# Performance work log

Measured on AMD Instinct MI355X. Metric: run time of the kernel, lower is better.

Reference implementation:

```python
import jax, jax.numpy as jnp
import numpy as np

B, L, SIZE, HEADS, AH, NBR, KER, DEPTH = 64, 512, 128, 8, 16, 15, 16, 3
MAXD = 20.0
N = B * L
EDGE = KER + 3 + 9 + 1  # 29


def _normalize(v):
    return v / (jnp.linalg.norm(v, axis=-1, keepdims=True) + 1e-8)


def _frames(pos):
    # local orientation frame per residue from consecutive CA displacements
    u = _normalize(pos[1:] - pos[:-1])            # (N-1,3)
    up = jnp.concatenate([u[:1], u], axis=0)      # u_{i-1}
    un = jnp.concatenate([u, u[-1:]], axis=0)     # u_i
    b = _normalize(up - un)
    n = _normalize(jnp.cross(up, un))
    return jnp.stack([b, n, jnp.cross(b, n)], axis=-1)  # (N,3,3)


def setup_inputs() -> dict:
    key = jax.random.key(0)
    ks = jax.random.split(key, 16)
    g = lambda i, shape, s=1.0: jax.random.normal(ks[i], shape, jnp.float32) * s
    return {
        "tertiary": g(0, (N, 3, 3), 10.0),
        "sequence": g(1, (N, 20)),
        "subgraph_indices": jnp.arange(N, dtype=jnp.int32) // L,
        "knn_noise": g(2, (B, L, L)),
        "embed_w": g(3, (27, SIZE), 0.1), "embed_b": jnp.zeros((SIZE,), jnp.float32),
        "wq": g(4, (DEPTH, SIZE, HEADS * AH), 0.08),
        "wk": g(5, (DEPTH, SIZE + EDGE, HEADS * AH), 0.08),
        "wv": g(6, (DEPTH, SIZE + EDGE, HEADS * AH), 0.08),
        "wo": g(7, (DEPTH, HEADS * AH, SIZE), 0.08),
        "mlp_w1": g(8, (DEPTH, SIZE, SIZE), 0.08), "mlp_b1": jnp.zeros((DEPTH, SIZE), jnp.float32),
        "mlp_w2": g(9, (DEPTH, SIZE, SIZE), 0.08), "mlp_b2": jnp.zeros((DEPTH, SIZE), jnp.float32),
        "mlp_w3": g(10, (DEPTH, SIZE, SIZE), 0.08), "mlp_b3": jnp.zeros((DEPTH, SIZE), jnp.float32),
        "pool_w": g(11, (4, SIZE, SIZE, 3), 0.05), "pool_b": jnp.zeros((4, SIZE), jnp.float32),
        "energy_w": g(12, (SIZE, 1), 0.1), "energy_b": jnp.zeros((1,), jnp.float32),
    }


def _forward(tertiary, sequence, knn_noise, embed_w, embed_b, wq, wk, wv, wo,
             mlp_w1, mlp_b1, mlp_w2, mlp_b2, mlp_w3, mlp_b3,
             pool_w, pool_b, energy_w, energy_b):
    pos = tertiary[:, 1]                                   # (N,3) CA positions
    R = _frames(pos)                                       # (N,3,3)
    # ---- kNN per contiguous protein group with noisy distances ----
    pg = pos.reshape(B, L, 3)
    dist = jnp.linalg.norm(pg[:, :, None] - pg[:, None, :], axis=-1)  # (B,L,L)
    closeness = -dist + 3.0 * knn_noise
    idx = jax.lax.top_k(closeness, NBR)[1]                 # (B,L,NBR) local
    nbr = (idx + (jnp.arange(B) * L)[:, None, None]).reshape(N, NBR)
    # ---- RBF relative encoding (RelativeStructure.message) ----
    dvec = pos[nbr] - pos[:, None]                         # (N,NBR,3)
    d = jnp.linalg.norm(dvec, axis=-1)                     # (N,NBR)
    mu = jnp.linspace(0.0, MAXD, KER)
    sigma = MAXD / KER
    rbf = jnp.exp(-(((d[..., None] - mu) / sigma) ** 2))   # (N,NBR,KER)
    dirs = jnp.einsum('nrc,nkr->nkc', R, dvec / (d[..., None] + 1e-8))
    relrot = jnp.einsum('nrc,nkrd->nkcd', R, R[nbr]).reshape(N, NBR, 9)
    ind = jnp.arange(N, dtype=tertiary.dtype)
    relind = (ind[nbr] - ind[:, None])[..., None]
    edge = jnp.concatenate([rbf, dirs, relrot, relind], axis=-1)  # (N,NBR,EDGE)
    # ---- structured graph-attention encoder ----
    h = jnp.ones((N, 27), tertiary.dtype) @ embed_w + embed_b
    inv_sqrt = 1.0 / np.sqrt(AH).astype(np.float32)
    for l in range(DEPTH):
        q = (h @ wq[l]).reshape(N, HEADS, AH)
        kv = jnp.concatenate([h[nbr], edge], axis=-1)      # (N,NBR,SIZE+EDGE)
        k = (kv @ wk[l]).reshape(N, NBR, HEADS, AH)
        v = (kv @ wv[l]).reshape(N, NBR, HEADS, AH)
        logits = jnp.einsum('nhd,nkhd->nhk', q, k) * inv_sqrt
        a = jax.nn.softmax(logits, axis=-1)
        o = jnp.einsum('nhk,nkhd->nhd', a, v).reshape(N, HEADS * AH) @ wo[l]
        h = h + o
        m = jax.nn.relu(h @ mlp_w1[l] + mlp_b1[l])
        m = jax.nn.relu(m @ mlp_w2[l] + mlp_b2[l])
        h = h + m @ mlp_w3[l] + mlp_b3[l]
    # ---- scatter-pad pool: residual conv + maxpool(2), x4, then length-sum ----
    x = h.reshape(B, L, SIZE).transpose(0, 2, 1)           # (B,SIZE,L)
    for i in range(4):
        y = jax.lax.conv_general_dilated(
            x, pool_w[i], (1,), ((1, 1),),
            dimension_numbers=('NCH', 'OIH', 'NCH')) + pool_b[i][None, :, None]
        x = x + jax.nn.leaky_relu(y, 0.01)
        Lc = x.shape[-1]
        x = x.reshape(B, SIZE, Lc // 2, 2).max(axis=-1)
    pooled = x.sum(axis=-1)                                # (B,SIZE)
    return pooled @ energy_w + energy_b                    # (B,1)


def reference(tertiary, sequence, subgraph_indices, knn_noise, embed_w, embed_b,
              wq, wk, wv, wo, mlp_w1, mlp_b1, mlp_w2, mlp_b2, mlp_w3, mlp_b3,
              pool_w, pool_b, energy_w, energy_b):
    # subgraph_indices encodes contiguous equal-size groups (arange // L)
    return _forward(tertiary, sequence, knn_noise, embed_w, embed_b, wq, wk, wv, wo,
                    mlp_w1, mlp_b1, mlp_w2, mlp_b2, mlp_w3, mlp_b3,
                    pool_w, pool_b, energy_w, energy_b)
```

## Files before the change

kernel.cpp:

```cpp
#include <hip/hip_runtime.h>
#include <math.h>

#define N_TOT 32768
#define NNBR 15
#define APW 8
#define ELPH 40
#define ETP 20
#define PLP 20

#define KNB 4096
#define FRB 128
#define PRB 3392

#define EB 1920

typedef __attribute__((ext_vector_type(8))) _Float16 f16x8;
typedef __attribute__((ext_vector_type(2))) _Float16 f16x2;
typedef __attribute__((ext_vector_type(4))) float f32x4;

#define CBAR() __asm__ volatile("" ::: "memory")
#define PAIR(v, c) __builtin_shufflevector(v, v, 2 * (c), 2 * (c) + 1)

__device__ __forceinline__ _Float16 f2h(float x) { return (_Float16)x; }

// ... 214 lines not shown
      int r = idx % 32768;
      int blk = r >> 14;
      int cout = (r >> 7) & 127;
      int jp = r & 127;
      int j = blk * 128 + jp;
      float val = 0.f;
      if (j < 232) {
        int e = j >> 3, hh = j & 7;
        const float* wvp = wv + (size_t)lL * 157 * 128 + (size_t)(128 + e) * 128 + hh * 16;
        const float* wop = wo + (size_t)lL * 16384 + (size_t)(hh * 16) * 128 + cout;
#pragma unroll
        for (int d = 0; d < 16; d++) val = fmaf(wvp[d], wop[d * 128], val);
      }
      wpe[(size_t)idx] = f2h(val);
    } else if (pb2 < 2880) {
      int idx = (pb2 - 2112) * 256 + tid;
      int kt = idx % 3;
      int rest = idx / 3;
      int i = rest % 128; rest /= 128;
      int oo = rest % 128;
      int s = rest / 128;
      wct[(((size_t)s * 3 + kt) * 128 + oo) * 128 + i] = f2h(pw[idx]);
    } else {
      int vb = pb2 - 2880;
      if (tid < 128) {
        float s = ebias[tid];
#pragma unroll
        for (int i = 0; i < 27; i++) s += ew[i * 128 + tid];
        hvS[tid] = s;
      }
      __syncthreads();
      size_t total = (size_t)N_TOT * 128;
      for (size_t j = (size_t)vb * 256 + tid; j < total; j += (size_t)512 * 256)
        h[j] = f2h(hvS[j & 127]);
    }
  }
}

template <int NTHR>
__device__ __forceinline__ void stage_w_async(const _Float16* __restrict__ W,
                                              _Float16* Ws, int tid) {
  int wv = tid >> 6, lane = tid & 63;
  constexpr int ITERS = 16384 / (NTHR * 8);
#pragma unroll
  for (int it = 0; it < ITERS; it++) {
    int base = it * (NTHR * 8) + wv * 512;
    int off = base + lane * 8;
    int row = off >> 7;
    int cL = (off >> 3) & 15;
    int cS = cL ^ (row & 7);
    const _Float16* src = W + ((size_t)row << 7) + (cS << 3);
    __builtin_amdgcn_global_load_lds(
        (const __attribute__((address_space(1))) void*)src,
        (__attribute__((address_space(3))) void*)(Ws + base), 16, 0, 0);
  }
}
template <int NTHR, int ROWS>
__device__ __forceinline__ void stage_x(const _Float16* __restrict__ src, _Float16* X,
                                        int tid, int rowstride) {
  for (int j = tid; j < ROWS * 16; j += NTHR) {
    int row = j >> 4, seg = (j & 15) * 8;
    *(uint4*)&X[row * 136 + seg] = *(const uint4*)(src + (size_t)row * rowstride + seg);
  }
}
template <bool RESET>
__device__ __forceinline__ void gemm_tile_t(const _Float16* X, const _Float16* Ws,
                                            int wrow, int l16, int quad, f32x4 acc[8]) {
  if (RESET) {
#pragma unroll
    for (int t = 0; t < 8; t++) acc[t] = (f32x4){0.f, 0.f, 0.f, 0.f};
  }
#pragma unroll
  for (int kk = 0; kk < 4; kk++) {
    f16x8 a = *(const f16x8*)&X[(wrow + l16) * 136 + kk * 32 + quad * 8];
#pragma unroll
    for (int t = 0; t < 8; t++) {
      int rw = t * 16 + l16;
      f16x8 b = *(const f16x8*)&Ws[(rw << 7) + ((((kk << 2) + quad) ^ (rw & 7)) << 3)];
      acc[t] = __builtin_amdgcn_mfma_f32_16x16x32_f16(a, b, acc[t], 0, 0, 0);
    }
  }
}

__global__ __launch_bounds__(256) void k_eq(const float* __restrict__ pos,
                                            const float* __restrict__ R,
                                            const int* __restrict__ nbr,
                                            _Float16* __restrict__ edge,
                                            const _Float16* __restrict__ A,
                                            const _Float16* __restrict__ Wqt,
                                            const _Float16* __restrict__ Wkt,
                                            const _Float16* __restrict__ Wvt,
                                            const _Float16* __restrict__ Wqk0,
                                            const _Float16* __restrict__ Wqk1,
                                            _Float16* __restrict__ q, _Float16* __restrict__ hk,
                                            _Float16* __restrict__ hv, _Float16* __restrict__ qkw) {
  __shared__ _Float16 X[64 * 136];
  __shared__ _Float16 Ws[128 * 128];
  int bb = blockIdx.x, tid = threadIdx.x;
  if (bb < EB) {
    int idx = bb * 256 + tid;
    if (idx >= N_TOT * NNBR) return;
    int n = idx / NNBR;
    int m = nbr[idx];
    float dx = pos[m * 3 + 0] - pos[n * 3 + 0];
    float dy = pos[m * 3 + 1] - pos[n * 3 + 1];
    float dz = pos[m * 3 + 2] - pos[n * 3 + 2];
    float d = sqrtf(dx * dx + dy * dy + dz * dz);
    _Float16 eb[32];
#pragma unroll
    for (int j = 0; j < 16; j++) {
      float mu = (20.f / 15.f) * (float)j;
      float t = (d - mu) * 0.8f;
      eb[j] = f2h(__expf(-t * t));
    }
    float inv = 1.f / (d + 1e-8f);
    float ux = dx * inv, uy = dy * inv, uz = dz * inv;
    float Rn[9], Rm[9];
#pragma unroll
    for (int j = 0; j < 9; j++) { Rn[j] = R[(size_t)n * 9 + j]; Rm[j] = R[(size_t)m * 9 + j]; }
#pragma unroll
    for (int cc = 0; cc < 3; cc++)
      eb[16 + cc] = f2h(Rn[0 * 3 + cc] * ux + Rn[1 * 3 + cc] * uy + Rn[2 * 3 + cc] * uz);
#pragma unroll
    for (int cc = 0; cc < 3; cc++)
#pragma unroll
      for (int dd = 0; dd < 3; dd++)
        eb[19 + cc * 3 + dd] = f2h(Rn[0 * 3 + cc] * Rm[0 * 3 + dd] +
                                   Rn[1 * 3 + cc] * Rm[1 * 3 + dd] +
                                   Rn[2 * 3 + cc] * Rm[2 * 3 + dd]);
    eb[28] = f2h((float)(m - n));
    eb[29] = (_Float16)0.f; eb[30] = (_Float16)0.f; eb[31] = (_Float16)0.f;
    _Float16* e = edge + (size_t)idx * 32;
#pragma unroll
    for (int v = 0; v < 4; v++)
      *(uint4*)(e + v * 8) = *(const uint4*)(&eb[v * 8]);
  } else {
    int r0 = (bb - EB) * 64;
    int lane = tid & 63, quad = lane >> 4, l16 = lane & 15, wrow = (tid >> 6) * 16;
    stage_x<256, 64>(A + (size_t)r0 * 128, X, tid, 128);
    const _Float16* wts[5] = {Wqt, Wkt, Wvt, Wqk0, Wqk1};
    f32x4 acc[8];
    for (int w = 0; w < 5; w++) {
      __syncthreads();
      stage_w_async<256>(wts[w], Ws, tid);
      __syncthreads();
      gemm_tile_t<true>(X, Ws, wrow, l16, quad, acc);
#pragma unroll
      for (int t = 0; t < 8; t++) {
        int col = t * 16 + l16;
#pragma unroll
        for (int r = 0; r < 4; r++) {
          float v = acc[t][r];
          int rowg = r0 + wrow + quad * 4 + r;
          if (w < 3) {
            _Float16* C = (w == 0) ? q : (w == 1) ? hk : hv;
            C[(size_t)rowg * 128 + col] = f2h(v);
          } else {
            qkw[(size_t)rowg * 256 + (w - 3) * 128 + col] = f2h(v);
          }
        }
      }
    }
  }
}

__global__ __launch_bounds__(256) void k_post(const _Float16* __restrict__ o,
                                              const _Float16* __restrict__ pe_g,
                                              _Float16* __restrict__ h,
                                              const _Float16* __restrict__ Wot,
                                              const _Float16* __restrict__ Wpe0,
                                              const _Float16* __restrict__ Wpe1,
                                              const _Float16* __restrict__ W1t, const float* __restrict__ B1,
                                              const _Float16* __restrict__ W2t, const float* __restrict__ B2,
                                              const _Float16* __restrict__ W3t, const float* __restrict__ B3,
                                              const _Float16* __restrict__ Wqt,
                                              const _Float16* __restrict__ Wkt,
                                              const _Float16* __restrict__ Wvt,
                                              const _Float16* __restrict__ Wqk0,
                                              const _Float16* __restrict__ Wqk1,
                                              _Float16* __restrict__ qo, _Float16* __restrict__ hko,
                                              _Float16* __restrict__ hvo, _Float16* __restrict__ qkwo,
                                              int do_qkv) {
  __shared__ _Float16 X[64 * 136];
  __shared__ _Float16 Ws[128 * 128];
  int tid = threadIdx.x, r0 = blockIdx.x * 64;
  int lane = tid & 63, quad = lane >> 4, l16 = lane & 15, wrow = (tid >> 6) * 16;
  f32x4 acc[8], hres[8];
  stage_x<256, 64>(o + (size_t)r0 * 128, X, tid, 128);
  stage_w_async<256>(Wot, Ws, tid);
  __syncthreads();
  gemm_tile_t<true>(X, Ws, wrow, l16, quad, acc);
  const _Float16* wpes[2] = {Wpe0, Wpe1};
#pragma unroll 1
  for (int blk = 0; blk < 2; blk++) {
    __syncthreads();
    stage_x<256, 64>(pe_g + (size_t)r0 * 256 + blk * 128, X, tid, 256);
    stage_w_async<256>(wpes[blk], Ws, tid);
    __syncthreads();
    gemm_tile_t<false>(X, Ws, wrow, l16, quad, acc);
  }
#pragma unroll
  for (int t = 0; t < 8; t++) {
    int col = t * 16 + l16;
#pragma unroll
    for (int r = 0; r < 4; r++)
      hres[t][r] = acc[t][r] + (float)h[(size_t)(r0 + wrow + quad * 4 + r) * 128 + col];
  }
  __syncthreads();
#pragma unroll
  for (int t = 0; t < 8; t++) {
    int col = t * 16 + l16;
#pragma unroll
    for (int r = 0; r < 4; r++)
      X[(wrow + quad * 4 + r) * 136 + col] = f2h(hres[t][r]);
  }
  stage_w_async<256>(W1t, Ws, tid);
  __syncthreads();
  gemm_tile_t<true>(X, Ws, wrow, l16, quad, acc);
  __syncthreads();
#pragma unroll
  for (int t = 0; t < 8; t++) {
    int col = t * 16 + l16; float bv = B1[col];
#pragma unroll
    for (int r = 0; r < 4; r++)
      X[(wrow + quad * 4 + r) * 136 + col] = f2h(fmaxf(acc[t][r] + bv, 0.f));
  }
  stage_w_async<256>(W2t, Ws, tid);
  __syncthreads();
  gemm_tile_t<true>(X, Ws, wrow, l16, quad, acc);
  __syncthreads();
#pragma unroll
  for (int t = 0; t < 8; t++) {
    int col = t * 16 + l16; float bv = B2[col];
#pragma unroll
    for (int r = 0; r < 4; r++)
      X[(wrow + quad * 4 + r) * 136 + col] = f2h(fmaxf(acc[t][r] + bv, 0.f));
  }
  stage_w_async<256>(W3t, Ws, tid);
  __syncthreads();
  gemm_tile_t<true>(X, Ws, wrow, l16, quad, acc);
  __syncthreads();
#pragma unroll
  for (int t = 0; t < 8; t++) {
    int col = t * 16 + l16; float bv = B3[col];
#pragma unroll
    for (int r = 0; r < 4; r++) {
      float v = hres[t][r] + acc[t][r] + bv;
      h[(size_t)(r0 + wrow + quad * 4 + r) * 128 + col] = f2h(v);
      if (do_qkv) X[(wrow + quad * 4 + r) * 136 + col] = f2h(v);
    }
  }
  if (!do_qkv) return;
  const _Float16* wts[5] = {Wqt, Wkt, Wvt, Wqk0, Wqk1};
  for (int w = 0; w < 5; w++) {
    __syncthreads();
    stage_w_async<256>(wts[w], Ws, tid);
    __syncthreads();
    gemm_tile_t<true>(X, Ws, wrow, l16, quad, acc);
#pragma unroll
    for (int t = 0; t < 8; t++) {
      int col = t * 16 + l16;
#pragma unroll
      for (int r = 0; r < 4; r++) {
        float v = acc[t][r];
        int rowg = r0 + wrow + quad * 4 + r;
        if (w < 3) {
          _Float16* C = (w == 0) ? qo : (w == 1) ? hko : hvo;
          C[(size_t)rowg * 128 + col] = f2h(v);
        } else {
          qkwo[(size_t)rowg * 256 + (w - 3) * 128 + col] = f2h(v);
        }
      }
    }
  }
}

__global__ __launch_bounds__(256) void k_attn(const _Float16* __restrict__ q,
                                              const _Float16* __restrict__ hk,
                                              const _Float16* __restrict__ hv,
                                              const int* __restrict__ nbr,
                                              const _Float16* __restrict__ edge,
                                              const _Float16* __restrict__ qkw,
                                              _Float16* __restrict__ o,
                                              _Float16* __restrict__ pe_g) {
  __shared__ _Float16 elL[4][15 * ELPH];
  __shared__ float etL[4][32 * ETP];
  __shared__ float plL[4][8 * PLP];
  __shared__ int nbL[4][16];
  int tid = threadIdx.x, wave = tid >> 6, lane = tid & 63;
  _Float16* el = elL[wave]; float* et = etL[wave]; float* pl = plL[wave];
  int* nbl = nbL[wave];
  int h8 = lane & 7, k2 = lane >> 3, c2 = lane * 2, h5 = lane >> 3;
  int kst = lane >> 2, gst = lane & 3;
  if (lane < 32) et[lane * ETP + 15] = 0.f;
  int n0 = (blockIdx.x * 4 + wave) * APW;
#pragma unroll 1
  for (int ni = 0; ni < APW; ni++) {
    int n = n0 + ni;
    if (lane < 60) {
      f16x8 ev = *(const f16x8*)(edge + ((size_t)n * 15 + kst) * 32 + gst * 8);
      *(f16x8*)&el[kst * ELPH + gst * 8] = ev;
      int ebs = gst * 8;
      et[(ebs + 0) * ETP + kst] = (float)ev[0];
      et[(ebs + 1) * ETP + kst] = (float)ev[1];
      et[(ebs + 2) * ETP + kst] = (float)ev[2];
      et[(ebs + 3) * ETP + kst] = (float)ev[3];
      et[(ebs + 4) * ETP + kst] = (float)ev[4];
      et[(ebs + 5) * ETP + kst] = (float)ev[5];
      et[(ebs + 6) * ETP + kst] = (float)ev[6];
      et[(ebs + 7) * ETP + kst] = (float)ev[7];
    }
    if (lane < 15) nbl[lane] = nbr[(size_t)n * NNBR + lane];
    const _Float16* qs = qkw + (size_t)n * 256 + h8 * 32;
    f16x8 w0 = *(const f16x8*)qs, w1 = *(const f16x8*)(qs + 8);
    f16x8 w2 = *(const f16x8*)(qs + 16), w3 = *(const f16x8*)(qs + 24);
    const _Float16* qp = q + (size_t)n * 128 + h8 * 16;
    f16x8 qa = *(const f16x8*)qp, qb = *(const f16x8*)(qp + 8);
    CBAR();
#pragma unroll
    for (int p = 0; p < 2; p++) {
      int k = k2 + p * 8;
      if (k < 15) {
        int m = nbl[k];
        const _Float16* hkp = hk + (size_t)m * 128 + h8 * 16;
        f16x8 ha = *(const f16x8*)hkp, hb = *(const f16x8*)(hkp + 8);
        float d0 = 0.f, d1 = 0.f;
        d0 = fdot2(PAIR(qa, 0), PAIR(ha, 0), d0);
        d1 = fdot2(PAIR(qa, 1), PAIR(ha, 1), d1);
        d0 = fdot2(PAIR(qa, 2), PAIR(ha, 2), d0);
        d1 = fdot2(PAIR(qa, 3), PAIR(ha, 3), d1);
        d0 = fdot2(PAIR(qb, 0), PAIR(hb, 0), d0);
        d1 = fdot2(PAIR(qb, 1), PAIR(hb, 1), d1);
        d0 = fdot2(PAIR(qb, 2), PAIR(hb, 2), d0);
        d1 = fdot2(PAIR(qb, 3), PAIR(hb, 3), d1);
        f16x8 l0 = *(const f16x8*)&el[k * ELPH + 0];
        f16x8 l1 = *(const f16x8*)&el[k * ELPH + 8];
        f16x8 l2 = *(const f16x8*)&el[k * ELPH + 16];
        f16x8 l3 = *(const f16x8*)&el[k * ELPH + 24];
        float e0 = 0.f, e1 = 0.f;
        e0 = fdot2(PAIR(l0, 0), PAIR(w0, 0), e0);
        e1 = fdot2(PAIR(l0, 1), PAIR(w0, 1), e1);
        e0 = fdot2(PAIR(l0, 2), PAIR(w0, 2), e0);
        e1 = fdot2(PAIR(l0, 3), PAIR(w0, 3), e1);
        e0 = fdot2(PAIR(l1, 0), PAIR(w1, 0), e0);
        e1 = fdot2(PAIR(l1, 1), PAIR(w1, 1), e1);
        e0 = fdot2(PAIR(l1, 2), PAIR(w1, 2), e0);
        e1 = fdot2(PAIR(l1, 3), PAIR(w1, 3), e1);
        e0 = fdot2(PAIR(l2, 0), PAIR(w2, 0), e0);
        e1 = fdot2(PAIR(l2, 1), PAIR(w2, 1), e1);
        e0 = fdot2(PAIR(l2, 2), PAIR(w2, 2), e0);
        e1 = fdot2(PAIR(l2, 3), PAIR(w2, 3), e1);
        e0 = fdot2(PAIR(l3, 0), PAIR(w3, 0), e0);
        e1 = fdot2(PAIR(l3, 1), PAIR(w3, 1), e1);
        e0 = fdot2(PAIR(l3, 2), PAIR(w3, 2), e0);
        e1 = fdot2(PAIR(l3, 3), PAIR(w3, 3), e1);
        pl[h8 * PLP + k] = fmaf(0.25f, d0 + d1, e0 + e1);
      } else {
        pl[h8 * PLP + 15] = -1e30f;
      }
    }
    CBAR();
    {
      int hh = lane >> 3, g = lane & 7;
      float va = pl[hh * PLP + g];
      float vb = pl[hh * PLP + 8 + g];
      float mx = fmaxf(va, vb);
      mx = fmaxf(mx, dpp_mov_f32<0xB1>(mx));
      mx = fmaxf(mx, dpp_mov_f32<0x4E>(mx));
      mx = fmaxf(mx, dpp_mov_f32<0x141>(mx));
      float ea = __expf(va - mx), eb = __expf(vb - mx);
      float s = ea + eb;
      s += dpp_mov_f32<0xB1>(s);
      s += dpp_mov_f32<0x4E>(s);
      s += dpp_mov_f32<0x141>(s);
      float inv = 1.f / s;
      pl[hh * PLP + g] = ea * inv;
      pl[hh * PLP + 8 + g] = eb * inv;
    }
    CBAR();
    _Float16* peo = pe_g + (size_t)n * 256;
#pragma unroll
    for (int p = 0; p < 4; p++) {
      int j = p * 64 + lane;
      float s = 0.f;
      if (j < 232) {
        int e = j >> 3, hh = j & 7;
        f32x4 p0 = *(const f32x4*)&pl[hh * PLP + 0];
        f32x4 p1 = *(const f32x4*)&pl[hh * PLP + 4];
        f32x4 p2 = *(const f32x4*)&pl[hh * PLP + 8];
        f32x4 p3 = *(const f32x4*)&pl[hh * PLP + 12];
        f32x4 t0 = *(const f32x4*)&et[e * ETP + 0];
        f32x4 t1 = *(const f32x4*)&et[e * ETP + 4];
        f32x4 t2 = *(const f32x4*)&et[e * ETP + 8];
        f32x4 t3 = *(const f32x4*)&et[e * ETP + 12];
        s = p0[0]*t0[0] + p0[1]*t0[1] + p0[2]*t0[2] + p0[3]*t0[3]
          + p1[0]*t1[0] + p1[1]*t1[1] + p1[2]*t1[2] + p1[3]*t1[3]
          + p2[0]*t2[0] + p2[1]*t2[1] + p2[2]*t2[2] + p2[3]*t2[3]
          + p3[0]*t3[0] + p3[1]*t3[1] + p3[2]*t3[2] + p3[3]*t3[3];
      }
      peo[j] = f2h(s);
    }
    float pk[16];
    *(f32x4*)&pk[0]  = *(const f32x4*)&pl[h5 * PLP + 0];
    *(f32x4*)&pk[4]  = *(const f32x4*)&pl[h5 * PLP + 4];
    *(f32x4*)&pk[8]  = *(const f32x4*)&pl[h5 * PLP + 8];
    *(f32x4*)&pk[12] = *(const f32x4*)&pl[h5 * PLP + 12];
    float ox = 0.f, oy = 0.f;
#pragma unroll
    for (int k = 0; k < 15; k++) {
      int m = nbl[k];
      f16x2 hh = *(const f16x2*)(hv + (size_t)m * 128 + c2);
      ox = fmaf(pk[k], (float)hh[0], ox);
      oy = fmaf(pk[k], (float)hh[1], oy);
    }
    *(f16x2*)(o + (size_t)n * 128 + c2) = (f16x2){f2h(ox), f2h(oy)};
    CBAR();
  }
}

__global__ __launch_bounds__(256) void k_convpool_m(const _Float16* __restrict__ x,
                                                    const _Float16* __restrict__ Wc,
                                                    const float* __restrict__ bias,
                                                    _Float16* __restrict__ outp, int Tin) {
  __shared__ _Float16 Xs[66 * 136];
  __shared__ _Float16 Ws[128 * 128];
  int tid = threadIdx.x;
  int b = blockIdx.y;
  int t0 = blockIdx.x * 64;
  for (int j = tid; j < 66 * 16; j += 256) {
    int row = j >> 4, seg = (j & 15) * 8;
    int t = t0 - 1 + row;
    uint4 v = {0u, 0u, 0u, 0u};
    if (t >= 0 && t < Tin) v = *(const uint4*)(x + ((size_t)b * Tin + t) * 128 + seg);
    *(uint4*)&Xs[row * 136 + seg] = v;
  }
  int lane = tid & 63, quad = lane >> 4, l16 = lane & 15, wrow = (tid >> 6) * 16;
  f32x4 acc[8];
#pragma unroll
  for (int t = 0; t < 8; t++) acc[t] = (f32x4){0.f, 0.f, 0.f, 0.f};
  for (int kt = 0; kt < 3; kt++) {
    __syncthreads();
    stage_w_async<256>(Wc + (size_t)kt * 16384, Ws, tid);
    __syncthreads();
#pragma unroll
    for (int kk = 0; kk < 4; kk++) {
      f16x8 a = *(const f16x8*)&Xs[(wrow + l16 + kt) * 136 + kk * 32 + quad * 8];
#pragma unroll
      for (int t = 0; t < 8; t++) {
        int rw = t * 16 + l16;
        f16x8 bfr = *(const f16x8*)&Ws[(rw << 7) + ((((kk << 2) + quad) ^ (rw & 7)) << 3)];
        acc[t] = __builtin_amdgcn_mfma_f32_16x16x32_f16(a, bfr, acc[t], 0, 0, 0);
      }
    }
  }
  int Tout = Tin >> 1;
#pragma unroll
  for (int t = 0; t < 8; t++) {
    int col = t * 16 + l16;
    float bv = bias[col];
#pragma unroll
    for (int rp = 0; rp < 2; rp++) {
      int rl0 = wrow + quad * 4 + rp * 2;
      float y0 = acc[t][rp * 2] + bv;
      float y1 = acc[t][rp * 2 + 1] + bv;
      float z0 = (float)Xs[(rl0 + 1) * 136 + col] + (y0 >= 0.f ? y0 : 0.01f * y0);
      float z1 = (float)Xs[(rl0 + 2) * 136 + col] + (y1 >= 0.f ? y1 : 0.01f * y1);
      outp[((size_t)b * Tout + ((t0 + rl0) >> 1)) * 128 + col] = f2h(fmaxf(z0, z1));
    }
  }
}

__global__ __launch_bounds__(128) void k_final(const _Float16* __restrict__ x,
                                               const float* __restrict__ ew,
                                               const float* __restrict__ ebb,
                                               float* __restrict__ outp) {
  int b = blockIdx.x, cc = threadIdx.x;
  float s = 0.f;
#pragma unroll
  for (int t = 0; t < 32; t++) s += (float)x[((size_t)b * 32 + t) * 128 + cc];
  float v = s * ew[cc];
#pragma unroll
  for (int m = 1; m < 64; m <<= 1) v += __shfl_xor(v, m);
  __shared__ float red[2];
  if ((cc & 63) == 0) red[cc >> 6] = v;
  __syncthreads();
  if (cc == 0) outp[b] = red[0] + red[1] + ebb[0];
}

extern "C" void kernel_launch(void* const* d_in, const int* in_sizes, int n_in,
                              void* d_out, int out_size, void* d_ws, size_t ws_size,
                              hipStream_t stream) {
  (void)in_sizes; (void)n_in; (void)out_size; (void)ws_size;
  const float* tert    = (const float*)d_in[0];
  const float* noise   = (const float*)d_in[3];
  const float* embed_w = (const float*)d_in[4];
  const float* embed_b = (const float*)d_in[5];
  const float* wq = (const float*)d_in[6];
  const float* wk = (const float*)d_in[7];
  const float* wv = (const float*)d_in[8];
  const float* wo = (const float*)d_in[9];
  const float* w1 = (const float*)d_in[10];
  const float* b1 = (const float*)d_in[11];
  const float* w2 = (const float*)d_in[12];
  const float* b2 = (const float*)d_in[13];
  const float* w3 = (const float*)d_in[14];
  const float* b3 = (const float*)d_in[15];
  const float* pw = (const float*)d_in[16];
  const float* pb = (const float*)d_in[17];
  const float* ew = (const float*)d_in[18];
  const float* eb = (const float*)d_in[19];
  float* outp = (float*)d_out;

  char* W = (char*)d_ws;
  float* pos  = (float*)W;        W += 393216;
  float* R    = (float*)W;        W += 1179648;
  int*   nbr  = (int*)W;          W += 1966080;
  _Float16* edge = (_Float16*)W;  W += 31457280;
  _Float16* h    = (_Float16*)W;  W += 8388608;
  _Float16* q    = (_Float16*)W;  W += 8388608;
  _Float16* hk   = (_Float16*)W;  W += 8388608;
  _Float16* hv   = (_Float16*)W;  W += 8388608;
  _Float16* o    = (_Float16*)W;  W += 8388608;
  _Float16* qkw_g = (_Float16*)W; W += 16777216;
  _Float16* pe_g  = (_Float16*)W; W += 16777216;
  _Float16* xa   = (_Float16*)W;  W += 4194304;
  _Float16* xb   = (_Float16*)W;  W += 2097152;
  _Float16* wbt  = (_Float16*)W;  W += 688128;
  _Float16* wqk  = (_Float16*)W;  W += 196608;
  _Float16* wpe  = (_Float16*)W;  W += 196608;
  _Float16* wct  = (_Float16*)W;  W += 393216;

  k_pre<<<KNB + FRB + PRB, 256, 0, stream>>>(tert, noise, nbr, pos, R,
                                             wq, wk, wv, wo, w1, w2, w3, wbt,
                                             wqk, wpe, pw, wct, embed_w, embed_b, h);

  const _Float16* wt[3][7];
  for (int l = 0; l < 3; l++)
    for (int w = 0; w < 7; w++) wt[l][w] = wbt + (size_t)(l * 7 + w) * 16384;
  const _Float16* wqk_l[3][2];
  const _Float16* wpe_l[3][2];
  for (int l = 0; l < 3; l++)
    for (int bk = 0; bk < 2; bk++) {
      wqk_l[l][bk] = wqk + (size_t)(l * 2 + bk) * 16384;
      wpe_l[l][bk] = wpe + (size_t)(l * 2 + bk) * 16384;
    }

  k_eq<<<EB + 512, 256, 0, stream>>>(pos, R, nbr, edge,
                                     h, wt[0][0], wt[0][1], wt[0][2],
                                     wqk_l[0][0], wqk_l[0][1], q, hk, hv, qkw_g);
  for (int l = 0; l < 3; l++) {
    k_attn<<<1024, 256, 0, stream>>>(q, hk, hv, nbr, edge, qkw_g, o, pe_g);
    int nl = l + 1;
    int do_qkv = (nl < 3) ? 1 : 0;
    k_post<<<512, 256, 0, stream>>>(o, pe_g, h, wt[l][3],
                                    wpe_l[l][0], wpe_l[l][1],
                                    wt[l][4], b1 + l * 128,
                                    wt[l][5], b2 + l * 128,
                                    wt[l][6], b3 + l * 128,
                                    do_qkv ? wt[nl][0] : nullptr,
                                    do_qkv ? wt[nl][1] : nullptr,
                                    do_qkv ? wt[nl][2] : nullptr,
                                    do_qkv ? wqk_l[nl][0] : nullptr,
                                    do_qkv ? wqk_l[nl][1] : nullptr,
                                    q, hk, hv, qkw_g, do_qkv);
  }

  k_convpool_m<<<dim3(8, 64), 256, 0, stream>>>(h,  wct + 0 * 49152, pb + 0,   xa, 512);
  k_convpool_m<<<dim3(4, 64), 256, 0, stream>>>(xa, wct + 1 * 49152, pb + 128, xb, 256);
  k_convpool_m<<<dim3(2, 64), 256, 0, stream>>>(xb, wct + 2 * 49152, pb + 256, xa, 128);
  k_convpool_m<<<dim3(1, 64), 256, 0, stream>>>(xa, wct + 3 * 49152, pb + 384, xb, 64);
  k_final<<<64, 128, 0, stream>>>(xb, ew, eb, outp);
}
```

Before: 449.6 us.

## Fuse attention into post-attention MLP kernel with double-buffered QKV

Adds a fused k_ap kernel in which each 64-row block first computes neighbor attention for its rows, placing the attention output straight into shared memory, then runs the output projection, MLP and next-layer QKV GEMMs. The q/hk/hv/qkw buffers are ping-ponged so that next-layer projections do not overwrite inputs still being read by other blocks. This removes one launch per layer and the global round trip of the attention output. In exchange, attention now runs on only 512 blocks, each wave handling 16 rows sequentially, which lowers parallelism. The fused path is used only when the workspace is large enough, otherwise the old two-kernel path runs.

Measured after the change: 461.4 us. 1.03x slower.

```diff
diff --git a/kernel.cpp b/kernel.cpp
--- a/kernel.cpp
+++ b/kernel.cpp
@@ -320,6 +320,240 @@
   }
 }
 
+__device__ __forceinline__ void attn_row(int n, int lane,
+                                         const _Float16* __restrict__ q,
+                                         const _Float16* __restrict__ hk,
+                                         const _Float16* __restrict__ hv,
+                                         const int* __restrict__ nbr,
+                                         const _Float16* __restrict__ edge,
+                                         const _Float16* __restrict__ qkw,
+                                         _Float16* __restrict__ pe_g,
+                                         _Float16* el, float* et, float* pl, int* nbl,
+                                         float& ox, float& oy) {
+  int h8 = lane & 7, k2 = lane >> 3, c2 = lane * 2, h5 = lane >> 3;
+  int kst = lane >> 2, gst = lane & 3;
+  if (lane < 60) {
+    f16x8 ev = *(const f16x8*)(edge + ((size_t)n * 15 + kst) * 32 + gst * 8);
+    *(f16x8*)&el[kst * ELPH + gst * 8] = ev;
+    int ebs = gst * 8;
+    et[(ebs + 0) * ETP + kst] = (float)ev[0];
+    et[(ebs + 1) * ETP + kst] = (float)ev[1];
+    et[(ebs + 2) * ETP + kst] = (float)ev[2];
+    et[(ebs + 3) * ETP + kst] = (float)ev[3];
+    et[(ebs + 4) * ETP + kst] = (float)ev[4];
+    et[(ebs + 5) * ETP + kst] = (float)ev[5];
+    et[(ebs + 6) * ETP + kst] = (float)ev[6];
+    et[(ebs + 7) * ETP + kst] = (float)ev[7];
+  }
+  if (lane < 15) nbl[lane] = nbr[(size_t)n * NNBR + lane];
+  const _Float16* qs = qkw + (size_t)n * 256 + h8 * 32;
+  f16x8 w0 = *(const f16x8*)qs, w1 = *(const f16x8*)(qs + 8);
+  f16x8 w2 = *(const f16x8*)(qs + 16), w3 = *(const f16x8*)(qs + 24);
+  const _Float16* qp = q + (size_t)n * 128 + h8 * 16;
+  f16x8 qa = *(const f16x8*)qp, qb = *(const f16x8*)(qp + 8);
+  CBAR();
+#pragma unroll
+  for (int p = 0; p < 2; p++) {
+    int k = k2 + p * 8;
+    if (k < 15) {
+      int m = nbl[k];
+      const _Float16* hkp = hk + (size_t)m * 128 + h8 * 16;
+      f16x8 ha = *(const f16x8*)hkp, hb = *(const f16x8*)(hkp + 8);
+      float d0 = 0.f, d1 = 0.f;
+      d0 = fdot2(PAIR(qa, 0), PAIR(ha, 0), d0);
+      d1 = fdot2(PAIR(qa, 1), PAIR(ha, 1), d1);
+      d0 = fdot2(PAIR(qa, 2), PAIR(ha, 2), d0);
+      d1 = fdot2(PAIR(qa, 3), PAIR(ha, 3), d1);
+      d0 = fdot2(PAIR(qb, 0), PAIR(hb, 0), d0);
+      d1 = fdot2(PAIR(qb, 1), PAIR(hb, 1), d1);
+      d0 = fdot2(PAIR(qb, 2), PAIR(hb, 2), d0);
+      d1 = fdot2(PAIR(qb, 3), PAIR(hb, 3), d1);
+      f16x8 l0 = *(const f16x8*)&el[k * ELPH + 0];
+      f16x8 l1 = *(const f16x8*)&el[k * ELPH + 8];
+      f16x8 l2 = *(const f16x8*)&el[k * ELPH + 16];
+      f16x8 l3 = *(const f16x8*)&el[k * ELPH + 24];
+      float e0 = 0.f, e1 = 0.f;
+      e0 = fdot2(PAIR(l0, 0), PAIR(w0, 0), e0);
+      e1 = fdot2(PAIR(l0, 1), PAIR(w0, 1), e1);
+      e0 = fdot2(PAIR(l0, 2), PAIR(w0, 2), e0);
+      e1 = fdot2(PAIR(l0, 3), PAIR(w0, 3), e1);
+      e0 = fdot2(PAIR(l1, 0), PAIR(w1, 0), e0);
+      e1 = fdot2(PAIR(l1, 1), PAIR(w1, 1), e1);
+      e0 = fdot2(PAIR(l1, 2), PAIR(w1, 2), e0);
+      e1 = fdot2(PAIR(l1, 3), PAIR(w1, 3), e1);
+      e0 = fdot2(PAIR(l2, 0), PAIR(w2, 0), e0);
+      e1 = fdot2(PAIR(l2, 1), PAIR(w2, 1), e1);
+      e0 = fdot2(PAIR(l2, 2), PAIR(w2, 2), e0);
+      e1 = fdot2(PAIR(l2, 3), PAIR(w2, 3), e1);
+      e0 = fdot2(PAIR(l3, 0), PAIR(w3, 0), e0);
+      e1 = fdot2(PAIR(l3, 1), PAIR(w3, 1), e1);
+      e0 = fdot2(PAIR(l3, 2), PAIR(w3, 2), e0);
+      e1 = fdot2(PAIR(l3, 3), PAIR(w3, 3), e1);
+      pl[h8 * PLP + k] = fmaf(0.25f, d0 + d1, e0 + e1);
+    } else {
+      pl[h8 * PLP + 15] = -1e30f;
+    }
+  }
+  CBAR();
+  {
+    int hh = lane >> 3, g = lane & 7;
+    float va = pl[hh * PLP + g];
+    float vb = pl[hh * PLP + 8 + g];
+    float mx = fmaxf(va, vb);
+    mx = fmaxf(mx, dpp_mov_f32<0xB1>(mx));
+    mx = fmaxf(mx, dpp_mov_f32<0x4E>(mx));
+    mx = fmaxf(mx, dpp_mov_f32<0x141>(mx));
+    float ea = __expf(va - mx), eb = __expf(vb - mx);
+    float s = ea + eb;
+    s += dpp_mov_f32<0xB1>(s);
+    s += dpp_mov_f32<0x4E>(s);
+    s += dpp_mov_f32<0x141>(s);
+    float inv = 1.f / s;
+    pl[hh * PLP + g] = ea * inv;
+    pl[hh * PLP + 8 + g] = eb * inv;
+  }
+  CBAR();
+  _Float16* peo = pe_g + (size_t)n * 256;
+#pragma unroll
+  for (int p = 0; p < 4; p++) {
+    int j = p * 64 + lane;
+    float s = 0.f;
+    if (j < 232) {
+      int e = j >> 3, hh = j & 7;
+      f32x4 p0 = *(const f32x4*)&pl[hh * PLP + 0];
+      f32x4 p1 = *(const f32x4*)&pl[hh * PLP + 4];
+      f32x4 p2 = *(const f32x4*)&pl[hh * PLP + 8];
+      f32x4 p3 = *(const f32x4*)&pl[hh * PLP + 12];
+      f32x4 t0 = *(const f32x4*)&et[e * ETP + 0];
+      f32x4 t1 = *(const f32x4*)&et[e * ETP + 4];
+      f32x4 t2 = *(const f32x4*)&et[e * ETP + 8];
+      f32x4 t3 = *(const f32x4*)&et[e * ETP + 12];
+      s = p0[0]*t0[0] + p0[1]*t0[1] + p0[2]*t0[2] + p0[3]*t0[3]
+        + p1[0]*t1[0] + p1[1]*t1[1] + p1[2]*t1[2] + p1[3]*t1[3]
+        + p2[0]*t2[0] + p2[1]*t2[1] + p2[2]*t2[2] + p2[3]*t2[3]
+        + p3[0]*t3[0] + p3[1]*t3[1] + p3[2]*t3[2] + p3[3]*t3[3];
+    }
+    peo[j] = f2h(s);
+  }
+  float pk[16];
+  *(f32x4*)&pk[0]  = *(const f32x4*)&pl[h5 * PLP + 0];
+  *(f32x4*)&pk[4]  = *(const f32x4*)&pl[h5 * PLP + 4];
+  *(f32x4*)&pk[8]  = *(const f32x4*)&pl[h5 * PLP + 8];
+  *(f32x4*)&pk[12] = *(const f32x4*)&pl[h5 * PLP + 12];
+  ox = 0.f; oy = 0.f;
+#pragma unroll
+  for (int k = 0; k < 15; k++) {
+    int m = nbl[k];
+    f16x2 hh2 = *(const f16x2*)(hv + (size_t)m * 128 + c2);
+    ox = fmaf(pk[k], (float)hh2[0], ox);
+    oy = fmaf(pk[k], (float)hh2[1], oy);
+  }
+  CBAR();
+}
+
+__device__ __forceinline__ void post_body(
+    const _Float16* __restrict__ pe_g, _Float16* __restrict__ h,
+    const _Float16* __restrict__ Wot, const _Float16* __restrict__ Wpe0,
+    const _Float16* __restrict__ Wpe1,
+    const _Float16* __restrict__ W1t, const float* __restrict__ B1,
+    const _Float16* __restrict__ W2t, const float* __restrict__ B2,
+    const _Float16* __restrict__ W3t, const float* __restrict__ B3,
+    const _Float16* __restrict__ Wqt, const _Float16* __restrict__ Wkt,
+    const _Float16* __restrict__ Wvt, const _Float16* __restrict__ Wqk0,
+    const _Float16* __restrict__ Wqk1,
+    _Float16* __restrict__ qo, _Float16* __restrict__ hko,
+    _Float16* __restrict__ hvo, _Float16* __restrict__ qkwo, int do_qkv,
+    _Float16* X, _Float16* Ws, int tid, int r0) {
+  int lane = tid & 63, quad = lane >> 4, l16 = lane & 15, wrow = (tid >> 6) * 16;
+  f32x4 acc[8], hres[8];
+  stage_w_async<256>(Wot, Ws, tid);
+  __syncthreads();
+  gemm_tile_t<true>(X, Ws, wrow, l16, quad, acc);
+  const _Float16* wpes[2] = {Wpe0, Wpe1};
+#pragma unroll 1
+  for (int blk = 0; blk < 2; blk++) {
+    __syncthreads();
+    stage_x<256, 64>(pe_g + (size_t)r0 * 256 + blk * 128, X, tid, 256);
+    stage_w_async<256>(wpes[blk], Ws, tid);
+    __syncthreads();
+    gemm_tile_t<false>(X, Ws, wrow, l16, quad, acc);
+  }
+#pragma unroll
+  for (int t = 0; t < 8; t++) {
+    int col = t * 16 + l16;
+#pragma unroll
+    for (int r = 0; r < 4; r++)
+      hres[t][r] = acc[t][r] + (float)h[(size_t)(r0 + wrow + quad * 4 + r) * 128 + col];
+  }
+  __syncthreads();
+#pragma unroll
+  for (int t = 0; t < 8; t++) {
+    int col = t * 16 + l16;
+#pragma unroll
+    for (int r = 0; r < 4; r++)
+      X[(wrow + quad * 4 + r) * 136 + col] = f2h(hres[t][r]);
+  }
+  stage_w_async<256>(W1t, Ws, tid);
+  __syncthreads();
+  gemm_tile_t<true>(X, Ws, wrow, l16, quad, acc);
+  __syncthreads();
+#pragma unroll
+  for (int t = 0; t < 8; t++) {
+    int col = t * 16 + l16; float bv = B1[col];
+#pragma unroll
+    for (int r = 0; r < 4; r++)
+      X[(wrow + quad * 4 + r) * 136 + col] = f2h(fmaxf(acc[t][r] + bv, 0.f));
+  }
+  stage_w_async<256>(W2t, Ws, tid);
+  __syncthreads();
+  gemm_tile_t<true>(X, Ws, wrow, l16, quad, acc);
+  __syncthreads();
+#pragma unroll
+  for (int t = 0; t < 8; t++) {
+    int col = t * 16 + l16; float bv = B2[col];
+#pragma unroll
+    for (int r = 0; r < 4; r++)
+      X[(wrow + quad * 4 + r) * 136 + col] = f2h(fmaxf(acc[t][r] + bv, 0.f));
+  }
+  stage_w_async<256>(W3t, Ws, tid);
+  __syncthreads();
+  gemm_tile_t<true>(X, Ws, wrow, l16, quad, acc);
+  __syncthreads();
+#pragma unroll
+  for (int t = 0; t < 8; t++) {
+    int col = t * 16 + l16; float bv = B3[col];
+#pragma unroll
+    for (int r = 0; r < 4; r++) {
+      float v = hres[t][r] + acc[t][r] + bv;
+      h[(size_t)(r0 + wrow + quad * 4 + r) * 128 + col] = f2h(v);
+      if (do_qkv) X[(wrow + quad * 4 + r) * 136 + col] = f2h(v);
+    }
+  }
+  if (!do_qkv) return;
+  const _Float16* wts[5] = {Wqt, Wkt, Wvt, Wqk0, Wqk1};
+  for (int w = 0; w < 5; w++) {
+    __syncthreads();
+    stage_w_async<256>(wts[w], Ws, tid);
+    __syncthreads();
+    gemm_tile_t<true>(X, Ws, wrow, l16, quad, acc);
+#pragma unroll
+    for (int t = 0; t < 8; t++) {
+      int col = t * 16 + l16;
+#pragma unroll
+      for (int r = 0; r < 4; r++) {
+        float v = acc[t][r];
+        int rowg = r0 + wrow + quad * 4 + r;
+        if (w < 3) {
+          _Float16* C = (w == 0) ? qo : (w == 1) ? hko : hvo;
+          C[(size_t)rowg * 128 + col] = f2h(v);
+        } else {
+          qkwo[(size_t)rowg * 256 + (w - 3) * 128 + col] = f2h(v);
+        }
+      }
+    }
+  }
+}
+
 __global__ __launch_bounds__(256) void k_eq(const float* __restrict__ pos,
                                             const float* __restrict__ R,
                                             const int* __restrict__ nbr,
@@ -402,6 +636,74 @@
   }
 }
 
+__global__ __launch_bounds__(256) void k_ap(
+    const _Float16* __restrict__ q, const _Float16* __restrict__ hk,
+    const _Float16* __restrict__ hv, const int* __restrict__ nbr,
+    const _Float16* __restrict__ edge, const _Float16* __restrict__ qkw,
+    _Float16* __restrict__ pe_g, _Float16* __restrict__ h,
+    const _Float16* __restrict__ Wot, const _Float16* __restrict__ Wpe0,
+    const _Float16* __restrict__ Wpe1,
+    const _Float16* __restrict__ W1t, const float* __restrict__ B1,
+    const _Float16* __restrict__ W2t, const float* __restrict__ B2,
+    const _Float16* __restrict__ W3t, const float* __restrict__ B3,
+    const _Float16* __restrict__ Wqt, const _Float16* __restrict__ Wkt,
+    const _Float16* __restrict__ Wvt, const _Float16* __restrict__ Wqk0,
+    const _Float16* __restrict__ Wqk1,
+    _Float16* __restrict__ qo, _Float16* __restrict__ hko,
+    _Float16* __restrict__ hvo, _Float16* __restrict__ qkwo, int do_qkv) {
+  __shared__ _Float16 X[64 * 136];
+  __shared__ _Float16 Ws[128 * 128];
+  int tid = threadIdx.x, wave = tid >> 6, lane = tid & 63;
+  int r0 = blockIdx.x * 64;
+  {
+    _Float16* el = Ws + wave * (15 * ELPH);
+    float* et = (float*)((char*)Ws + 4800) + wave * (32 * ETP);
+    float* pl = (float*)((char*)Ws + 15040) + wave * (8 * PLP);
+    int* nbl = (int*)((char*)Ws + 17600) + wave * 16;
+    int c2 = lane * 2;
+    if (lane < 32) et[lane * ETP + 15] = 0.f;
+    int n0 = r0 + wave * 16;
+#pragma unroll 1
+    for (int ni = 0; ni < 16; ni++) {
+      float ox, oy;
+      attn_row(n0 + ni, lane, q, hk, hv, nbr, edge, qkw, pe_g,
+               el, et, pl, nbl, ox, oy);
+      *(f16x2*)&X[(wave * 16 + ni) * 136 + c2] = (f16x2){f2h(ox), f2h(oy)};
+    }
+  }
+  __syncthreads();
+  post_body(pe_g, h, Wot, Wpe0, Wpe1, W1t, B1, W2t, B2, W3t, B3,
+            Wqt, Wkt, Wvt, Wqk0, Wqk1, qo, hko, hvo, qkwo, do_qkv,
+            X, Ws, tid, r0);
+}
+
+__global__ __launch_bounds__(256) void k_attn(const _Float16* __restrict__ q,
+                                              const _Float16* __restrict__ hk,
+                                              const _Float16* __restrict__ hv,
+                                              const int* __restrict__ nbr,
+                                              const _Float16* __restrict__ edge,
+                                              const _Float16* __restrict__ qkw,
+                                              _Float16* __restrict__ o,
+                                              _Float16* __restrict__ pe_g) {
+  __shared__ _Float16 elL[4][15 * ELPH];
+  __shared__ float etL[4][32 * ETP];
+  __shared__ float plL[4][8 * PLP];
+  __shared__ int nbL[4][16];
+  int tid = threadIdx.x, wave = tid >> 6, lane = tid & 63;
+  _Float16* el = elL[wave]; float* et = etL[wave]; float* pl = plL[wave];
+  int* nbl = nbL[wave];
+  int c2 = lane * 2;
+  if (lane < 32) et[lane * ETP + 15] = 0.f;
+  int n0 = (blockIdx.x * 4 + wave) * APW;
+#pragma unroll 1
+  for (int ni = 0; ni < APW; ni++) {
+    int n = n0 + ni;
+    float ox, oy;
+    attn_row(n, lane, q, hk, hv, nbr, edge, qkw, pe_g, el, et, pl, nbl, ox, oy);
+    *(f16x2*)(o + (size_t)n * 128 + c2) = (f16x2){f2h(ox), f2h(oy)};
+  }
+}
+
 __global__ __launch_bounds__(256) void k_post(const _Float16* __restrict__ o,
                                               const _Float16* __restrict__ pe_g,
                                               _Float16* __restrict__ h,
@@ -422,238 +724,10 @@
   __shared__ _Float16 X[64 * 136];
   __shared__ _Float16 Ws[128 * 128];
   int tid = threadIdx.x, r0 = blockIdx.x * 64;
-  int lane = tid & 63, quad = lane >> 4, l16 = lane & 15, wrow = (tid >> 6) * 16;
-  f32x4 acc[8], hres[8];
   stage_x<256, 64>(o + (size_t)r0 * 128, X, tid, 128);
-  stage_w_async<256>(Wot, Ws, tid);
-  __syncthreads();
-  gemm_tile_t<true>(X, Ws, wrow, l16, quad, acc);
-  const _Float16* wpes[2] = {Wpe0, Wpe1};
-#pragma unroll 1
-  for (int blk = 0; blk < 2; blk++) {
-    __syncthreads();
-    stage_x<256, 64>(pe_g + (size_t)r0 * 256 + blk * 128, X, tid, 256);
-    stage_w_async<256>(wpes[blk], Ws, tid);
-    __syncthreads();
-    gemm_tile_t<false>(X, Ws, wrow, l16, quad, acc);
-  }
-#pragma unroll
-  for (int t = 0; t < 8; t++) {
-    int col = t * 16 + l16;
-#pragma unroll
-    for (int r = 0; r < 4; r++)
-      hres[t][r] = acc[t][r] + (float)h[(size_t)(r0 + wrow + quad * 4 + r) * 128 + col];
-  }
-  __syncthreads();
-#pragma unroll
-  for (int t = 0; t < 8; t++) {
-    int col = t * 16 + l16;
-#pragma unroll
-    for (int r = 0; r < 4; r++)
-      X[(wrow + quad * 4 + r) * 136 + col] = f2h(hres[t][r]);
-  }
-  stage_w_async<256>(W1t, Ws, tid);
-  __syncthreads();
-  gemm_tile_t<true>(X, Ws, wrow, l16, quad, acc);
-  __syncthreads();
-#pragma unroll
-  for (int t = 0; t < 8; t++) {
-    int col = t * 16 + l16; float bv = B1[col];
-#pragma unroll
-    for (int r = 0; r < 4; r++)
-      X[(wrow + quad * 4 + r) * 136 + col] = f2h(fmaxf(acc[t][r] + bv, 0.f));
-  }
-  stage_w_async<256>(W2t, Ws, tid);
-  __syncthreads();
-  gemm_tile_t<true>(X, Ws, wrow, l16, quad, acc);
-  __syncthreads();
-#pragma unroll
-  for (int t = 0; t < 8; t++) {
-    int col = t * 16 + l16; float bv = B2[col];
-#pragma unroll
-    for (int r = 0; r < 4; r++)
-      X[(wrow + quad * 4 + r) * 136 + col] = f2h(fmaxf(acc[t][r] + bv, 0.f));
-  }
-  stage_w_async<256>(W3t, Ws, tid);
-  __syncthreads();
-  gemm_tile_t<true>(X, Ws, wrow, l16, quad, acc);
-  __syncthreads();
-#pragma unroll
-  for (int t = 0; t < 8; t++) {
-    int col = t * 16 + l16; float bv = B3[col];
-#pragma unroll
-    for (int r = 0; r < 4; r++) {
-      float v = hres[t][r] + acc[t][r] + bv;
-      h[(size_t)(r0 + wrow + quad * 4 + r) * 128 + col] = f2h(v);
-      if (do_qkv) X[(wrow + quad * 4 + r) * 136 + col] = f2h(v);
-    }
-  }
-  if (!do_qkv) return;
-  const _Float16* wts[5] = {Wqt, Wkt, Wvt, Wqk0, Wqk1};
-  for (int w = 0; w < 5; w++) {
-    __syncthreads();
-    stage_w_async<256>(wts[w], Ws, tid);
-    __syncthreads();
-    gemm_tile_t<true>(X, Ws, wrow, l16, quad, acc);
-#pragma unroll
-    for (int t = 0; t < 8; t++) {
-      int col = t * 16 + l16;
-#pragma unroll
-      for (int r = 0; r < 4; r++) {
-        float v = acc[t][r];
-        int rowg = r0 + wrow + quad * 4 + r;
-        if (w < 3) {
-          _Float16* C = (w == 0) ? qo : (w == 1) ? hko : hvo;
-          C[(size_t)rowg * 128 + col] = f2h(v);
-        } else {
-          qkwo[(size_t)rowg * 256 + (w - 3) * 128 + col] = f2h(v);
-        }
-      }
-    }
-  }
-}
-
-__global__ __launch_bounds__(256) void k_attn(const _Float16* __restrict__ q,
-                                              const _Float16* __restrict__ hk,
-                                              const _Float16* __restrict__ hv,
-                                              const int* __restrict__ nbr,
-                                              const _Float16* __restrict__ edge,
-                                              const _Float16* __restrict__ qkw,
-                                              _Float16* __restrict__ o,
-                                              _Float16* __restrict__ pe_g) {
-  __shared__ _Float16 elL[4][15 * ELPH];
-  __shared__ float etL[4][32 * ETP];
-  __shared__ float plL[4][8 * PLP];
-  __shared__ int nbL[4][16];
-  int tid = threadIdx.x, wave = tid >> 6, lane = tid & 63;
-  _Float16* el = elL[wave]; float* et = etL[wave]; float* pl = plL[wave];
-  int* nbl = nbL[wave];
-  int h8 = lane & 7, k2 = lane >> 3, c2 = lane * 2, h5 = lane >> 3;
-  int kst = lane >> 2, gst = lane & 3;
-  if (lane < 32) et[lane * ETP + 15] = 0.f;
-  int n0 = (blockIdx.x * 4 + wave) * APW;
-#pragma unroll 1
-  for (int ni = 0; ni < APW; ni++) {
-    int n = n0 + ni;
-    if (lane < 60) {
-      f16x8 ev = *(const f16x8*)(edge + ((size_t)n * 15 + kst) * 32 + gst * 8);
-      *(f16x8*)&el[kst * ELPH + gst * 8] = ev;
-      int ebs = gst * 8;
-      et[(ebs + 0) * ETP + kst] = (float)ev[0];
-      et[(ebs + 1) * ETP + kst] = (float)ev[1];
-      et[(ebs + 2) * ETP + kst] = (float)ev[2];
-      et[(ebs + 3) * ETP + kst] = (float)ev[3];
-      et[(ebs + 4) * ETP + kst] = (float)ev[4];
-      et[(ebs + 5) * ETP + kst] = (float)ev[5];
-      et[(ebs + 6) * ETP + kst] = (float)ev[6];
-      et[(ebs + 7) * ETP + kst] = (float)ev[7];
-    }
-    if (lane < 15) nbl[lane] = nbr[(size_t)n * NNBR + lane];
-    const _Float16* qs = qkw + (size_t)n * 256 + h8 * 32;
-    f16x8 w0 = *(const f16x8*)qs, w1 = *(const f16x8*)(qs + 8);
-    f16x8 w2 = *(const f16x8*)(qs + 16), w3 = *(const f16x8*)(qs + 24);
-    const _Float16* qp = q + (size_t)n * 128 + h8 * 16;
-    f16x8 qa = *(const f16x8*)qp, qb = *(const f16x8*)(qp + 8);
-    CBAR();
-#pragma unroll
-    for (int p = 0; p < 2; p++) {
-      int k = k2 + p * 8;
-      if (k < 15) {
-        int m = nbl[k];
-        const _Float16* hkp = hk + (size_t)m * 128 + h8 * 16;
-        f16x8 ha = *(const f16x8*)hkp, hb = *(const f16x8*)(hkp + 8);
-        float d0 = 0.f, d1 = 0.f;
-        d0 = fdot2(PAIR(qa, 0), PAIR(ha, 0), d0);
-        d1 = fdot2(PAIR(qa, 1), PAIR(ha, 1), d1);
-        d0 = fdot2(PAIR(qa, 2), PAIR(ha, 2), d0);
-        d1 = fdot2(PAIR(qa, 3), PAIR(ha, 3), d1);
-        d0 = fdot2(PAIR(qb, 0), PAIR(hb, 0), d0);
-        d1 = fdot2(PAIR(qb, 1), PAIR(hb, 1), d1);
-        d0 = fdot2(PAIR(qb, 2), PAIR(hb, 2), d0);
-        d1 = fdot2(PAIR(qb, 3), PAIR(hb, 3), d1);
-        f16x8 l0 = *(const f16x8*)&el[k * ELPH + 0];
-        f16x8 l1 = *(const f16x8*)&el[k * ELPH + 8];
-        f16x8 l2 = *(const f16x8*)&el[k * ELPH + 16];
-        f16x8 l3 = *(const f16x8*)&el[k * ELPH + 24];
-        float e0 = 0.f, e1 = 0.f;
-        e0 = fdot2(PAIR(l0, 0), PAIR(w0, 0), e0);
-        e1 = fdot2(PAIR(l0, 1), PAIR(w0, 1), e1);
-        e0 = fdot2(PAIR(l0, 2), PAIR(w0, 2), e0);
-        e1 = fdot2(PAIR(l0, 3), PAIR(w0, 3), e1);
-        e0 = fdot2(PAIR(l1, 0), PAIR(w1, 0), e0);
-        e1 = fdot2(PAIR(l1, 1), PAIR(w1, 1), e1);
-        e0 = fdot2(PAIR(l1, 2), PAIR(w1, 2), e0);
-        e1 = fdot2(PAIR(l1, 3), PAIR(w1, 3), e1);
-        e0 = fdot2(PAIR(l2, 0), PAIR(w2, 0), e0);
-        e1 = fdot2(PAIR(l2, 1), PAIR(w2, 1), e1);
-        e0 = fdot2(PAIR(l2, 2), PAIR(w2, 2), e0);
-        e1 = fdot2(PAIR(l2, 3), PAIR(w2, 3), e1);
-        e0 = fdot2(PAIR(l3, 0), PAIR(w3, 0), e0);
-        e1 = fdot2(PAIR(l3, 1), PAIR(w3, 1), e1);
-        e0 = fdot2(PAIR(l3, 2), PAIR(w3, 2), e0);
-        e1 = fdot2(PAIR(l3, 3), PAIR(w3, 3), e1);
-        pl[h8 * PLP + k] = fmaf(0.25f, d0 + d1, e0 + e1);
-      } else {
-        pl[h8 * PLP + 15] = -1e30f;
-      }
-    }
-    CBAR();
-    {
-      int hh = lane >> 3, g = lane & 7;
-      float va = pl[hh * PLP + g];
-      float vb = pl[hh * PLP + 8 + g];
-      float mx = fmaxf(va, vb);
-      mx = fmaxf(mx, dpp_mov_f32<0xB1>(mx));
-      mx = fmaxf(mx, dpp_mov_f32<0x4E>(mx));
-      mx = fmaxf(mx, dpp_mov_f32<0x141>(mx));
-      float ea = __expf(va - mx), eb = __expf(vb - mx);
-      float s = ea + eb;
-      s += dpp_mov_f32<0xB1>(s);
-      s += dpp_mov_f32<0x4E>(s);
-      s += dpp_mov_f32<0x141>(s);
-      float inv = 1.f / s;
-      pl[hh * PLP + g] = ea * inv;
-      pl[hh * PLP + 8 + g] = eb * inv;
-    }
-    CBAR();
-    _Float16* peo = pe_g + (size_t)n * 256;
-#pragma unroll
-    for (int p = 0; p < 4; p++) {
-      int j = p * 64 + lane;
-      float s = 0.f;
-      if (j < 232) {
-        int e = j >> 3, hh = j & 7;
-        f32x4 p0 = *(const f32x4*)&pl[hh * PLP + 0];
-        f32x4 p1 = *(const f32x4*)&pl[hh * PLP + 4];
-        f32x4 p2 = *(const f32x4*)&pl[hh * PLP + 8];
-        f32x4 p3 = *(const f32x4*)&pl[hh * PLP + 12];
-        f32x4 t0 = *(const f32x4*)&et[e * ETP + 0];
-        f32x4 t1 = *(const f32x4*)&et[e * ETP + 4];
-        f32x4 t2 = *(const f32x4*)&et[e * ETP + 8];
-        f32x4 t3 = *(const f32x4*)&et[e * ETP + 12];
-        s = p0[0]*t0[0] + p0[1]*t0[1] + p0[2]*t0[2] + p0[3]*t0[3]
-          + p1[0]*t1[0] + p1[1]*t1[1] + p1[2]*t1[2] + p1[3]*t1[3]
-          + p2[0]*t2[0] + p2[1]*t2[1] + p2[2]*t2[2] + p2[3]*t2[3]
-          + p3[0]*t3[0] + p3[1]*t3[1] + p3[2]*t3[2] + p3[3]*t3[3];
-      }
-      peo[j] = f2h(s);
-    }
-    float pk[16];
-    *(f32x4*)&pk[0]  = *(const f32x4*)&pl[h5 * PLP + 0];
-    *(f32x4*)&pk[4]  = *(const f32x4*)&pl[h5 * PLP + 4];
-    *(f32x4*)&pk[8]  = *(const f32x4*)&pl[h5 * PLP + 8];
-    *(f32x4*)&pk[12] = *(const f32x4*)&pl[h5 * PLP + 12];
-    float ox = 0.f, oy = 0.f;
-#pragma unroll
-    for (int k = 0; k < 15; k++) {
-      int m = nbl[k];
-      f16x2 hh = *(const f16x2*)(hv + (size_t)m * 128 + c2);
-      ox = fmaf(pk[k], (float)hh[0], ox);
-      oy = fmaf(pk[k], (float)hh[1], oy);
-    }
-    *(f16x2*)(o + (size_t)n * 128 + c2) = (f16x2){f2h(ox), f2h(oy)};
-    CBAR();
-  }
+  post_body(pe_g, h, Wot, Wpe0, Wpe1, W1t, B1, W2t, B2, W3t, B3,
+            Wqt, Wkt, Wvt, Wqk0, Wqk1, qo, hko, hvo, qkwo, do_qkv,
+            X, Ws, tid, r0);
 }
 
 __global__ __launch_bounds__(256) void k_convpool_m(const _Float16* __restrict__ x,
@@ -728,7 +802,7 @@
 extern "C" void kernel_launch(void* const* d_in, const int* in_sizes, int n_in,
                               void* d_out, int out_size, void* d_ws, size_t ws_size,
                               hipStream_t stream) {
-  (void)in_sizes; (void)n_in; (void)out_size; (void)ws_size;
+  (void)in_sizes; (void)n_in; (void)out_size;
   const float* tert    = (const float*)d_in[0];
   const float* noise   = (const float*)d_in[3];
   const float* embed_w = (const float*)d_in[4];
@@ -767,6 +841,12 @@
   _Float16* wqk  = (_Float16*)W;  W += 196608;
   _Float16* wpe  = (_Float16*)W;  W += 196608;
   _Float16* wct  = (_Float16*)W;  W += 393216;
+  _Float16* q2   = (_Float16*)W;  W += 8388608;
+  _Float16* hk2  = (_Float16*)W;  W += 8388608;
+  _Float16* hv2  = (_Float16*)W;  W += 8388608;
+  _Float16* qkw2 = (_Float16*)W;  W += 16777216;
+  size_t needed = (size_t)(W - (char*)d_ws);
+  int fused = (ws_size >= needed) ? 1 : 0;
 
   k_pre<<<KNB + FRB + PRB, 256, 0, stream>>>(tert, noise, nbr, pos, R,
                                              wq, wk, wv, wo, w1, w2, w3, wbt,
@@ -786,21 +866,46 @@
   k_eq<<<EB + 512, 256, 0, stream>>>(pos, R, nbr, edge,
                                      h, wt[0][0], wt[0][1], wt[0][2],
                                      wqk_l[0][0], wqk_l[0][1], q, hk, hv, qkw_g);
-  for (int l = 0; l < 3; l++) {
-    k_attn<<<1024, 256, 0, stream>>>(q, hk, hv, nbr, edge, qkw_g, o, pe_g);
-    int nl = l + 1;
-    int do_qkv = (nl < 3) ? 1 : 0;
-    k_post<<<512, 256, 0, stream>>>(o, pe_g, h, wt[l][3],
-                                    wpe_l[l][0], wpe_l[l][1],
+
+  if (fused) {
+    for (int l = 0; l < 3; l++) {
+      const _Float16 *qi, *hki, *hvi, *qkwi;
+      _Float16 *qoB, *hkoB, *hvoB, *qkwoB;
+      if (l & 1) { qi = q2; hki = hk2; hvi = hv2; qkwi = qkw2;
+                   qoB = q; hkoB = hk; hvoB = hv; qkwoB = qkw_g; }
+      else       { qi = q;  hki = hk;  hvi = hv;  qkwi = qkw_g;
+                   qoB = q2; hkoB = hk2; hvoB = hv2; qkwoB = qkw2; }
+      int nl = l + 1;
+      int do_qkv = (nl < 3) ? 1 : 0;
+      k_ap<<<512, 256, 0, stream>>>(qi, hki, hvi, nbr, edge, qkwi, pe_g, h,
+                                    wt[l][3], wpe_l[l][0], wpe_l[l][1],
                                     wt[l][4], b1 + l * 128,
                                     wt[l][5], b2 + l * 128,
                                     wt[l][6], b3 + l * 128,
-                                    do_qkv ? wt[nl][0] : nullptr,
-                                    do_qkv ? wt[nl][1] : nullptr,
-                                    do_qkv ? wt[nl][2] : nullptr,
-                                    do_qkv ? wqk_l[nl][0] : nullptr,
-                                    do_qkv ? wqk_l[nl][1] : nullptr,
-                                    q, hk, hv, qkw_g, do_qkv);
+                                    do_qkv ? wt[nl][0] : wt[0][0],
+                                    do_qkv ? wt[nl][1] : wt[0][1],
+                                    do_qkv ? wt[nl][2] : wt[0][2],
+                                    do_qkv ? wqk_l[nl][0] : wqk_l[0][0],
+                                    do_qkv ? wqk_l[nl][1] : wqk_l[0][1],
+                                    qoB, hkoB, hvoB, qkwoB, do_qkv);
+    }
+  } else {
+    for (int l = 0; l < 3; l++) {
+      k_attn<<<1024, 256, 0, stream>>>(q, hk, hv, nbr, edge, qkw_g, o, pe_g);
+      int nl = l + 1;
+      int do_qkv = (nl < 3) ? 1 : 0;
+      k_post<<<512, 256, 0, stream>>>(o, pe_g, h, wt[l][3],
+                                      wpe_l[l][0], wpe_l[l][1],
+                                      wt[l][4], b1 + l * 128,
+                                      wt[l][5], b2 + l * 128,
+                                      wt[l][6], b3 + l * 128,
+                                      do_qkv ? wt[nl][0] : wt[0][0],
+                                      do_qkv ? wt[nl][1] : wt[0][1],
+                                      do_qkv ? wt[nl][2] : wt[0][2],
+                                      do_qkv ? wqk_l[nl][0] : wqk_l[0][0],
+                                      do_qkv ? wqk_l[nl][1] : wqk_l[0][1],
+                                      q, hk, hv, qkw_g, do_qkv);
+    }
   }
 
   k_convpool_m<<<dim3(8, 64), 256, 0, stream>>>(h,  wct + 0 * 49152, pb + 0,   xa, 512);
```
